# Performance work log

Measured on AMD Instinct MI355X. Metric: run time of the kernel, lower is better.

Reference implementation:

```python
import jax, jax.numpy as jnp
import numpy as np

N_NODES = 50000
N_EDGES = 800000
IN_CH = 128
HID = 64
HEADS = 4
OUT_CH = 10
N_GRAPHS = 512
NEG_SLOPE = 0.2


def setup_inputs() -> dict:
    key = jax.random.key(0)
    ks = jax.random.split(key, 16)
    x = jax.random.normal(ks[0], (N_NODES, IN_CH), dtype=jnp.float32)
    edge_index = jax.random.randint(ks[1], (2, N_EDGES), 0, N_NODES, dtype=jnp.int64)
    batch = jnp.sort(jax.random.randint(ks[2], (N_NODES,), 0, N_GRAPHS, dtype=jnp.int64))
    s = 1.0 / np.sqrt(IN_CH)
    W1 = jax.random.uniform(ks[3], (IN_CH, HEADS * HID), jnp.float32, -s, s)
    att_src1 = jax.random.normal(ks[4], (HEADS, HID), jnp.float32) * 0.1
    att_dst1 = jax.random.normal(ks[5], (HEADS, HID), jnp.float32) * 0.1
    b1 = jnp.zeros((HEADS * HID,), jnp.float32)
    s2 = 1.0 / np.sqrt(HEADS * HID)
    W2 = jax.random.uniform(ks[6], (HEADS * HID, HID), jnp.float32, -s2, s2)
    att_src2 = jax.random.normal(ks[7], (1, HID), jnp.float32) * 0.1
    att_dst2 = jax.random.normal(ks[8], (1, HID), jnp.float32) * 0.1
    b2 = jnp.zeros((HID,), jnp.float32)
    s3 = 1.0 / np.sqrt(HID)
    Wl = jax.random.uniform(ks[9], (HID, OUT_CH), jnp.float32, -s3, s3)
    bl = jnp.zeros((OUT_CH,), jnp.float32)
    return dict(x=x, edge_index=edge_index, batch=batch,
                W1=W1, att_src1=att_src1, att_dst1=att_dst1, b1=b1,
                W2=W2, att_src2=att_src2, att_dst2=att_dst2, b2=b2,
                Wl=Wl, bl=bl)


def gat_conv(x, src, dst, W, att_src, att_dst, bias, heads, out_ch, concat):
    """PyG GATConv: gather -> per-edge attention -> segment softmax over dst -> scatter-add."""
    n = x.shape[0]
    h = (x @ W).reshape(n, heads, out_ch)            # [N,H,C]
    a_s = jnp.sum(h * att_src, axis=-1)              # [N,H]
    a_d = jnp.sum(h * att_dst, axis=-1)              # [N,H]
    e = jax.nn.leaky_relu(a_s[src] + a_d[dst], NEG_SLOPE)  # [E,H]
    m = jax.ops.segment_max(e, dst, num_segments=n)  # stable softmax per dst
    alpha = jnp.exp(e - m[dst])
    denom = jax.ops.segment_sum(alpha, dst, num_segments=n)
    alpha = alpha / denom[dst]
    out = jax.ops.segment_sum(h[src] * alpha[:, :, None], dst, num_segments=n)  # [N,H,C]
    if concat:
        out = out.reshape(n, heads * out_ch)
    else:
        out = out.mean(axis=1)
    return out + bias


def reference(x, edge_index, batch, W1, att_src1, att_dst1, b1,
              W2, att_src2, att_dst2, b2, Wl, bl):
    n = x.shape[0]
    # PyG GATConv default add_self_loops=True
    loops = jnp.arange(n, dtype=edge_index.dtype)
    src = jnp.concatenate([edge_index[0], loops])
    dst = jnp.concatenate([edge_index[1], loops])

    h = jax.nn.elu(gat_conv(x, src, dst, W1, att_src1, att_dst1, b1, HEADS, HID, True))
    h = jax.nn.elu(gat_conv(h, src, dst, W2, att_src2, att_dst2, b2, 1, HID, False))

    # global_mean_pool
    sums = jax.ops.segment_sum(h, batch, num_segments=N_GRAPHS)
    cnts = jax.ops.segment_sum(jnp.ones((n,), h.dtype), batch, num_segments=N_GRAPHS)
    pooled = sums / jnp.maximum(cnts, 1.0)[:, None]

    return pooled @ Wl + bl
```

## Files before the change

kernel.cpp:

```cpp
#include <hip/hip_runtime.h>
#include <hip/hip_bf16.h>
#include <math.h>

#define N_NODES 50000
#define N_EDGES 800000
#define IN_CH 128
#define HID 64
#define HEADS 4
#define OUT_CH 10
#define N_GRAPHS 512
#define NEG_SLOPE 0.2f

#define ETOT_C (N_EDGES + N_NODES)
#define GB1 ((N_NODES + 63) / 64)
#define GH  ((ETOT_C / 4 + 255) / 256)
#define GZ  32

using short8_t = __attribute__((ext_vector_type(8))) short;
using f32x4 = __attribute__((ext_vector_type(4))) float;

__device__ __forceinline__ float b2f(unsigned short u) {
    return __uint_as_float(((unsigned)u) << 16);
}
__device__ __forceinline__ unsigned short f2b(float f) {
    __hip_bfloat16 b = __float2bfloat16(f);
    return *(unsigned short*)&b;
}
__device__ __forceinline__ short f2bs(float f) {
    __hip_bfloat16 b = __float2bfloat16(f);
    return *(short*)&b;
}
__device__ __forceinline__ float lrelu(float x) { return x > 0.f ? x : NEG_SLOPE * x; }

__global__ void convw_k(const float* __restrict__ W1, const float* __restrict__ W2,
                        unsigned short* __restrict__ Wt1, unsigned short* __restrict__ Wt2) {
    int idx = blockIdx.x * 256 + threadIdx.x;
    if (idx < 256 * 128) {
        int n = idx / 128, k = idx % 128;
        Wt1[idx] = f2b(W1[(size_t)k * 256 + n]);
    }
    int j = idx - 256 * 128;
    if (j >= 0 && j < 64 * 256) {
        int n = j / 256, k = j % 256;
        Wt2[j] = f2b(W2[(size_t)k * 64 + n]);
    }
}

__global__ __launch_bounds__(256) void mega1_k(
        const float* __restrict__ X, const unsigned short* __restrict__ Wt,
        unsigned short* __restrict__ Yb,
        const float* __restrict__ asrc, const float* __restrict__ adst,
        float* __restrict__ As, float* __restrict__ Ad, int M,
        const int* __restrict__ dst, int* __restrict__ deg, int* __restrict__ rank,
        const int* __restrict__ batch, float* __restrict__ cntf,
        float* __restrict__ pooled) {
    int b = blockIdx.x;
    if (b < GB1) {
        const int lane = threadIdx.x & 63;
        const int w = threadIdx.x >> 6;
        const int r0 = b * 64 + w * 16;
        const int l15 = lane & 15;
        const int rc = min(r0 + l15, M - 1);
        const int kg = (lane >> 4) * 8;

        f32x4 acc[16] = {};
#pragma unroll
        for (int kc = 0; kc < 4; kc++) {
            int k0 = kc * 32 + kg;
            float4 xa = *(const float4*)&X[(size_t)rc * 128 + k0];
            float4 xb = *(const float4*)&X[(size_t)rc * 128 + k0 + 4];
            short8_t af;
            af[0] = f2bs(xa.x); af[1] = f2bs(xa.y); af[2] = f2bs(xa.z); af[3] = f2bs(xa.w);
            af[4] = f2bs(xb.x); af[5] = f2bs(xb.y); af[6] = f2bs(xb.z); af[7] = f2bs(xb.w);
#pragma unroll
            for (int ct = 0; ct < 16; ct++) {
                int col = ct * 16 + l15;
                short8_t bf = *(const short8_t*)&Wt[(size_t)col * 128 + k0];
                acc[ct] = __builtin_amdgcn_mfma_f32_16x16x32_bf16(af, bf, acc[ct], 0, 0, 0);
            }
        }

        const int rbase = r0 + (lane >> 4) * 4;
#pragma unroll
        for (int reg = 0; reg < 4; reg++) {
            int gr = rbase + reg;
            float s0 = 0.f, s1 = 0.f, s2 = 0.f, s3 = 0.f;
            float d0 = 0.f, d1 = 0.f, d2 = 0.f, d3 = 0.f;
#pragma unroll
            for (int cg = 0; cg < 4; cg++) {
                int c = cg * 16 + l15;
                float v0 = acc[0 * 4 + cg][reg], v1 = acc[1 * 4 + cg][reg];
                float v2 = acc[2 * 4 + cg][reg], v3 = acc[3 * 4 + cg][reg];
                s0 += v0 * asrc[0 * 64 + c]; d0 += v0 * adst[0 * 64 + c];
                s1 += v1 * asrc[1 * 64 + c]; d1 += v1 * adst[1 * 64 + c];
                s2 += v2 * asrc[2 * 64 + c]; d2 += v2 * adst[2 * 64 + c];
                s3 += v3 * asrc[3 * 64 + c]; d3 += v3 * adst[3 * 64 + c];
            }
#pragma unroll
            for (int o = 8; o > 0; o >>= 1) {
                s0 += __shfl_xor(s0, o); d0 += __shfl_xor(d0, o);
                s1 += __shfl_xor(s1, o); d1 += __shfl_xor(d1, o);
                s2 += __shfl_xor(s2, o); d2 += __shfl_xor(d2, o);
                s3 += __shfl_xor(s3, o); d3 += __shfl_xor(d3, o);
            }
            if (l15 == 0 && gr < M) {
                *(float4*)&As[gr * 4] = make_float4(s0, s1, s2, s3);
                *(float4*)&Ad[gr * 4] = make_float4(d0, d1, d2, d3);
            }
        }
#pragma unroll
        for (int reg = 0; reg < 4; reg++) {
            int gr = rbase + reg;
            if (gr >= M) continue;
#pragma unroll
            for (int cg = 0; cg < 4; cg++) {
                int c = cg * 16 + l15;
                ushort4 p;
                p.x = f2b(acc[0 * 4 + cg][reg]);
                p.y = f2b(acc[1 * 4 + cg][reg]);
                p.z = f2b(acc[2 * 4 + cg][reg]);
                p.w = f2b(acc[3 * 4 + cg][reg]);
                *(ushort4*)&Yb[(size_t)gr * 256 + c * 4] = p;
            }
        }
        return;
    }
    b -= GB1;
    if (b < GH) {
        const int nth = GH * 256;
        int i0 = b * 256 + threadIdx.x;
        int i1 = i0 + nth, i2 = i0 + 2 * nth, i3 = i0 + 3 * nth;
        bool v0 = i0 < ETOT_C, v1 = i1 < ETOT_C, v2 = i2 < ETOT_C, v3 = i3 < ETOT_C;
        int d0 = 0, d1 = 0, d2 = 0, d3 = 0;
        if (v0) d0 = (i0 < N_EDGES) ? dst[i0] : i0 - N_EDGES;
        if (v1) d1 = (i1 < N_EDGES) ? dst[i1] : i1 - N_EDGES;
        if (v2) d2 = (i2 < N_EDGES) ? dst[i2] : i2 - N_EDGES;
        if (v3) d3 = (i3 < N_EDGES) ? dst[i3] : i3 - N_EDGES;
        int r0 = 0, r1 = 0, r2 = 0, r3 = 0;
        if (v0) r0 = atomicAdd(&deg[d0], 1);
        if (v1) r1 = atomicAdd(&deg[d1], 1);
        if (v2) r2 = atomicAdd(&deg[d2], 1);
        if (v3) r3 = atomicAdd(&deg[d3], 1);
        if (v0) rank[i0] = r0;
        if (v1) rank[i1] = r1;
        if (v2) rank[i2] = r2;
        if (v3) rank[i3] = r3;
        return;
    }
    b -= GH;
    if (b < 2) {
        int g = b * 256 + threadIdx.x;
        if (g >= N_GRAPHS) return;
        int lo = 0, hi = N_NODES;
        while (lo < hi) { int mid = (lo + hi) >> 1; if (batch[mid] < g) lo = mid + 1; else hi = mid; }
        int lo2 = lo, hi2 = N_NODES;
        while (lo2 < hi2) { int mid = (lo2 + hi2) >> 1; if (batch[mid] < g + 1) lo2 = mid + 1; else hi2 = mid; }
        cntf[g] = (float)(lo2 - lo);
        return;
    }
    b -= 2;
    int idx = b * 256 + threadIdx.x;
    *(float4*)&pooled[(size_t)idx * 4] = make_float4(0.f, 0.f, 0.f, 0.f);
}

__global__ __launch_bounds__(256) void mfma_gemm2_k(
        const unsigned short* __restrict__ Xb, const unsigned short* __restrict__ Wt,
        unsigned short* __restrict__ Yb,
        const float* __restrict__ asrc, const float* __restrict__ adst,
        float* __restrict__ As, float* __restrict__ Ad, int M) {
    const int lane = threadIdx.x & 63;
    const int w = threadIdx.x >> 6;
    const int r0 = blockIdx.x * 64 + w * 16;
    const int l15 = lane & 15;
    const int rc = min(r0 + l15, M - 1);
    const int kg = (lane >> 4) * 8;

    f32x4 acc[4] = {};
#pragma unroll
    for (int kc = 0; kc < 8; kc++) {
        int k0 = kc * 32 + kg;
        short8_t af = *(const short8_t*)&Xb[(size_t)rc * 256 + k0];
#pragma unroll
        for (int ct = 0; ct < 4; ct++) {
            int col = ct * 16 + l15;
            short8_t bf = *(const short8_t*)&Wt[(size_t)col * 256 + k0];
            acc[ct] = __builtin_amdgcn_mfma_f32_16x16x32_bf16(af, bf, acc[ct], 0, 0, 0);
        }
    }

    const int rbase = r0 + (lane >> 4) * 4;
#pragma unroll
    for (int reg = 0; reg < 4; reg++) {
        int gr = rbase + reg;
        float sv = 0.f, dv = 0.f;
#pragma unroll
        for (int ct = 0; ct < 4; ct++) {
            int c = ct * 16 + l15;
            float v = acc[ct][reg];
            sv += v * asrc[c];
            dv += v * adst[c];
        }
#pragma unroll
        for (int o = 8; o > 0; o >>= 1) { sv += __shfl_xor(sv, o); dv += __shfl_xor(dv, o); }
        if (l15 == 0 && gr < M) { As[gr] = sv; Ad[gr] = dv; }
        if (gr < M) {
#pragma unroll
            for (int ct = 0; ct < 4; ct++)
                Yb[(size_t)gr * 64 + ct * 16 + l15] = f2b(acc[ct][reg]);
        }
    }
}

__global__ void blksum_k(const int* __restrict__ deg, int* __restrict__ bsum, int n) {
    int t = threadIdx.x;
    int i = blockIdx.x * 256 + t;
    int v = (i < n) ? deg[i] : 0;
#pragma unroll
    for (int o = 32; o > 0; o >>= 1) v += __shfl_xor(v, o);
    __shared__ int wsum[4];
    if ((t & 63) == 0) wsum[t >> 6] = v;
    __syncthreads();
    if (t == 0) bsum[blockIdx.x] = wsum[0] + wsum[1] + wsum[2] + wsum[3];
}

__global__ void scanb_k(int* __restrict__ bsum, int nb) {
    __shared__ int tmp[256];
    int t = threadIdx.x;
    int v = (t < nb) ? bsum[t] : 0;
    tmp[t] = v;
    __syncthreads();
    for (int o = 1; o < 256; o <<= 1) {
        int u = (t >= o) ? tmp[t - o] : 0;
        __syncthreads();
        tmp[t] += u;
        __syncthreads();
    }
    if (t < nb) bsum[t] = tmp[t] - v;
}

__global__ void scanapply_k(const int* __restrict__ deg, const int* __restrict__ bsum,
                            int* __restrict__ rowptr, int n) {
    __shared__ int tmp[256];
    int t = threadIdx.x;
    int i = blockIdx.x * 256 + t;
    int v = (i < n) ? deg[i] : 0;
    tmp[t] = v;
    __syncthreads();
    for (int o = 1; o < 256; o <<= 1) {
        int u = (t >= o) ? tmp[t - o] : 0;
        __syncthreads();
        tmp[t] += u;
        __syncthreads();
    }
    int boff = bsum[blockIdx.x];
    if (i < n) rowptr[i] = boff + tmp[t] - v;
    if (i == n - 1) rowptr[n] = boff + tmp[t];
}

__global__ void scatter_k(const int* __restrict__ src, const int* __restrict__ dst,
                          const int* __restrict__ rowptr, const int* __restrict__ rank,
                          int* __restrict__ csrc, int etot) {
    int i = blockIdx.x * blockDim.x + threadIdx.x;
    if (i >= etot) return;
    int s, d;
    if (i < N_EDGES) { s = src[i]; d = dst[i]; } else { s = d = i - N_EDGES; }
    csrc[rowptr[d] + rank[i]] = s;
}

__global__ void agg1_k(const int* __restrict__ rowptr, const int* __restrict__ csrc,
                       const float* __restrict__ As, const float* __restrict__ Ad,
                       const __hip_bfloat16* __restrict__ Hb,
                       const float* __restrict__ bias,
                       unsigned short* __restrict__ Outb, int nnodes) {
    __shared__ int ssh[4][64];
    __shared__ float4 wsh[4][64];
    int lane = threadIdx.x & 63;
    int w = threadIdx.x >> 6;
    int node = blockIdx.x * 4 + w;
    int beg = rowptr[node], end = rowptr[node + 1];
    int deg = end - beg;
    const unsigned short* hb = (const unsigned short*)Hb;
    float4 bv = *(const float4*)&Ad[node * 4];
    bool fast = (deg <= 64);
    if (fast) {
        bool act = lane < deg;
        int s = act ? csrc[beg + lane] : 0;
        float4 a = *(const float4*)&As[s * 4];
        float e0 = lrelu(a.x + bv.x), e1 = lrelu(a.y + bv.y);
        float e2 = lrelu(a.z + bv.z), e3 = lrelu(a.w + bv.w);
        if (!act) { e0 = e1 = e2 = e3 = -INFINITY; }
        float m0 = e0, m1 = e1, m2 = e2, m3 = e3;
#pragma unroll
        for (int o = 32; o > 0; o >>= 1) {
            m0 = fmaxf(m0, __shfl_xor(m0, o)); m1 = fmaxf(m1, __shfl_xor(m1, o));
            m2 = fmaxf(m2, __shfl_xor(m2, o)); m3 = fmaxf(m3, __shfl_xor(m3, o));
        }
        float x0 = act ? __expf(e0 - m0) : 0.f;
        float x1 = act ? __expf(e1 - m1) : 0.f;
        float x2 = act ? __expf(e2 - m2) : 0.f;
        float x3 = act ? __expf(e3 - m3) : 0.f;
        float d0 = x0, d1 = x1, d2 = x2, d3 = x3;
#pragma unroll
        for (int o = 32; o > 0; o >>= 1) {
            d0 += __shfl_xor(d0, o); d1 += __shfl_xor(d1, o);
            d2 += __shfl_xor(d2, o); d3 += __shfl_xor(d3, o);
        }
        ssh[w][lane] = s;
        wsh[w][lane] = make_float4(x0 / d0, x1 / d1, x2 / d2, x3 / d3);
    }
    __syncthreads();
    float acc0 = 0.f, acc1 = 0.f, acc2 = 0.f, acc3 = 0.f;
    if (fast) {
        float p0 = 0.f, p1 = 0.f, p2 = 0.f, p3 = 0.f;
        int j = 0;
        for (; j + 4 <= deg; j += 4) {
            int sA = ssh[w][j], sB = ssh[w][j + 1], sC = ssh[w][j + 2], sD = ssh[w][j + 3];
            float4 wA = wsh[w][j], wB = wsh[w][j + 1], wC = wsh[w][j + 2], wD = wsh[w][j + 3];
            ushort4 vA = *(const ushort4*)&hb[(size_t)sA * 256 + lane * 4];
            ushort4 vB = *(const ushort4*)&hb[(size_t)sB * 256 + lane * 4];
            ushort4 vC = *(const ushort4*)&hb[(size_t)sC * 256 + lane * 4];
            ushort4 vD = *(const ushort4*)&hb[(size_t)sD * 256 + lane * 4];
            acc0 += wA.x * b2f(vA.x) + wC.x * b2f(vC.x);
            p0   += wB.x * b2f(vB.x) + wD.x * b2f(vD.x);
            acc1 += wA.y * b2f(vA.y) + wC.y * b2f(vC.y);
            p1   += wB.y * b2f(vB.y) + wD.y * b2f(vD.y);
            acc2 += wA.z * b2f(vA.z) + wC.z * b2f(vC.z);
            p2   += wB.z * b2f(vB.z) + wD.z * b2f(vD.z);
            acc3 += wA.w * b2f(vA.w) + wC.w * b2f(vC.w);
            p3   += wB.w * b2f(vB.w) + wD.w * b2f(vD.w);
        }
        for (; j < deg; j++) {
            int s = ssh[w][j];
            float4 wt = wsh[w][j];
            ushort4 v = *(const ushort4*)&hb[(size_t)s * 256 + lane * 4];
            acc0 += wt.x * b2f(v.x); acc1 += wt.y * b2f(v.y);
            acc2 += wt.z * b2f(v.z); acc3 += wt.w * b2f(v.w);
        }
        acc0 += p0; acc1 += p1; acc2 += p2; acc3 += p3;
    } else {
        float m0 = -INFINITY, m1 = -INFINITY, m2 = -INFINITY, m3 = -INFINITY;
        for (int j = beg + lane; j < end; j += 64) {
            float4 a = *(const float4*)&As[csrc[j] * 4];
            m0 = fmaxf(m0, lrelu(a.x + bv.x)); m1 = fmaxf(m1, lrelu(a.y + bv.y));
            m2 = fmaxf(m2, lrelu(a.z + bv.z)); m3 = fmaxf(m3, lrelu(a.w + bv.w));
        }
#pragma unroll
        for (int o = 32; o > 0; o >>= 1) {
            m0 = fmaxf(m0, __shfl_xor(m0, o)); m1 = fmaxf(m1, __shfl_xor(m1, o));
            m2 = fmaxf(m2, __shfl_xor(m2, o)); m3 = fmaxf(m3, __shfl_xor(m3, o));
        }
        float d0 = 0.f, d1 = 0.f, d2 = 0.f, d3 = 0.f;
        for (int j = beg + lane; j < end; j += 64) {
            float4 a = *(const float4*)&As[csrc[j] * 4];
            d0 += __expf(lrelu(a.x + bv.x) - m0); d1 += __expf(lrelu(a.y + bv.y) - m1);
            d2 += __expf(lrelu(a.z + bv.z) - m2); d3 += __expf(lrelu(a.w + bv.w) - m3);
        }
#pragma unroll
        for (int o = 32; o > 0; o >>= 1) {
            d0 += __shfl_xor(d0, o); d1 += __shfl_xor(d1, o);
            d2 += __shfl_xor(d2, o); d3 += __shfl_xor(d3, o);
        }
        for (int j = beg; j < end; j++) {
            int s = csrc[j];
            float4 a = *(const float4*)&As[s * 4];
            float w0 = __expf(lrelu(a.x + bv.x) - m0) / d0;
            float w1 = __expf(lrelu(a.y + bv.y) - m1) / d1;
            float w2 = __expf(lrelu(a.z + bv.z) - m2) / d2;
            float w3 = __expf(lrelu(a.w + bv.w) - m3) / d3;
            ushort4 v = *(const ushort4*)&hb[(size_t)s * 256 + lane * 4];
            acc0 += w0 * b2f(v.x); acc1 += w1 * b2f(v.y);
            acc2 += w2 * b2f(v.z); acc3 += w3 * b2f(v.w);
        }
    }
    float r0 = acc0 + bias[0 * 64 + lane];
    float r1 = acc1 + bias[1 * 64 + lane];
    float r2 = acc2 + bias[2 * 64 + lane];
    float r3 = acc3 + bias[3 * 64 + lane];
    r0 = r0 > 0.f ? r0 : expm1f(r0);
    r1 = r1 > 0.f ? r1 : expm1f(r1);
    r2 = r2 > 0.f ? r2 : expm1f(r2);
    r3 = r3 > 0.f ? r3 : expm1f(r3);
    size_t base = (size_t)node * 256;
    Outb[base + 0 * 64 + lane] = f2b(r0);
    Outb[base + 1 * 64 + lane] = f2b(r1);
    Outb[base + 2 * 64 + lane] = f2b(r2);
    Outb[base + 3 * 64 + lane] = f2b(r3);
}

__global__ void agg2_k(const int* __restrict__ rowptr, const int* __restrict__ csrc,
                       const float* __restrict__ As, const float* __restrict__ Ad,
                       const __hip_bfloat16* __restrict__ Hb,
                       const float* __restrict__ bias, const int* __restrict__ batch,
                       float* __restrict__ pooled, int nnodes) {
    __shared__ int ssh[4][64];
    __shared__ float wsh[4][64];
    int lane = threadIdx.x & 63;
    int w = threadIdx.x >> 6;
    int node = blockIdx.x * 4 + w;
    int beg = rowptr[node], end = rowptr[node + 1];
    int deg = end - beg;
    const unsigned short* hb = (const unsigned short*)Hb;
    float ad = Ad[node];
    bool fast = (deg <= 64);
    if (fast) {
        bool act = lane < deg;
        int s = act ? csrc[beg + lane] : 0;
        float e = lrelu(As[s] + ad);
        if (!act) e = -INFINITY;
        float m = e;
#pragma unroll
        for (int o = 32; o > 0; o >>= 1) m = fmaxf(m, __shfl_xor(m, o));
        float x = act ? __expf(e - m) : 0.f;
        float d = x;
#pragma unroll
        for (int o = 32; o > 0; o >>= 1) d += __shfl_xor(d, o);
        ssh[w][lane] = s;
        wsh[w][lane] = x / d;
    }
    __syncthreads();
    float acc = 0.f;
    if (fast) {
        float p = 0.f;
        int j = 0;
        for (; j + 4 <= deg; j += 4) {
            int sA = ssh[w][j], sB = ssh[w][j + 1], sC = ssh[w][j + 2], sD = ssh[w][j + 3];
            float wA = wsh[w][j], wB = wsh[w][j + 1], wC = wsh[w][j + 2], wD = wsh[w][j + 3];
            acc += wA * b2f(hb[(size_t)sA * 64 + lane]) + wC * b2f(hb[(size_t)sC * 64 + lane]);
            p   += wB * b2f(hb[(size_t)sB * 64 + lane]) + wD * b2f(hb[(size_t)sD * 64 + lane]);
        }
        for (; j < deg; j++) acc += wsh[w][j] * b2f(hb[(size_t)ssh[w][j] * 64 + lane]);
        acc += p;
    } else {
        float m = -INFINITY;
        for (int j = beg + lane; j < end; j += 64) m = fmaxf(m, lrelu(As[csrc[j]] + ad));
#pragma unroll
        for (int o = 32; o > 0; o >>= 1) m = fmaxf(m, __shfl_xor(m, o));
        float d = 0.f;
        for (int j = beg + lane; j < end; j += 64) d += __expf(lrelu(As[csrc[j]] + ad) - m);
#pragma unroll
        for (int o = 32; o > 0; o >>= 1) d += __shfl_xor(d, o);
        for (int j = beg; j < end; j++) {
            int s = csrc[j];
            float wt = __expf(lrelu(As[s] + ad) - m) / d;
            acc += wt * b2f(hb[(size_t)s * 64 + lane]);
        }
    }
    float v = acc + bias[lane];
    v = v > 0.f ? v : expm1f(v);
    atomicAdd(&pooled[batch[node] * 64 + lane], v);
}

__global__ void final_k(const float* __restrict__ pooled, const float* __restrict__ cnt,
                        const float* __restrict__ Wl, const float* __restrict__ bl,
                        float* __restrict__ out) {
    int g = blockIdx.x;
    int t = threadIdx.x;
    __shared__ float s[64];
    float c = cnt[g];
    c = c > 1.f ? c : 1.f;
    s[t] = pooled[g * 64 + t] / c;
    __syncthreads();
    if (t < OUT_CH) {
        float acc = bl[t];
        for (int k = 0; k < 64; k++) acc += s[k] * Wl[k * OUT_CH + t];
        out[g * OUT_CH + t] = acc;
    }
}

extern "C" void kernel_launch(void* const* d_in, const int* in_sizes, int n_in,
                              void* d_out, int out_size, void* d_ws, size_t ws_size,
                              hipStream_t stream) {
    const float* x    = (const float*)d_in[0];
    const int*   ei   = (const int*)d_in[1];
    const int*   batch= (const int*)d_in[2];
    const float* W1   = (const float*)d_in[3];
    const float* as1  = (const float*)d_in[4];
    const float* ad1  = (const float*)d_in[5];
    const float* b1   = (const float*)d_in[6];
    const float* W2   = (const float*)d_in[7];
    const float* as2  = (const float*)d_in[8];
    const float* ad2  = (const float*)d_in[9];
    const float* b2   = (const float*)d_in[10];
    const float* Wl   = (const float*)d_in[11];
    const float* bl   = (const float*)d_in[12];
    float* out = (float*)d_out;

    const int* src = ei;
    const int* dst = ei + N_EDGES;
    const int ETOT = ETOT_C;
    const int NB = (N_NODES + 255) / 256;

    char* ws = (char*)d_ws;
    size_t off = 0;
    auto alloc = [&](size_t bytes) {
        void* p = ws + off;
        off = (off + bytes + 255) & ~((size_t)255);
        return p;
    };
    unsigned short* h1b  = (unsigned short*)alloc((size_t)N_NODES * 256 * 2);
    unsigned short* out1b= (unsigned short*)alloc((size_t)N_NODES * 256 * 2);
    float* As1    = (float*)alloc((size_t)N_NODES * 4 * 4);
    float* Ad1    = (float*)alloc((size_t)N_NODES * 4 * 4);
    float* As2    = (float*)alloc((size_t)N_NODES * 4);
    float* Ad2    = (float*)alloc((size_t)N_NODES * 4);
    int*   deg    = (int*)  alloc((size_t)N_NODES * 4);
    int*   rowptr = (int*)  alloc((size_t)(N_NODES + 1) * 4);
    int*   csrc   = (int*)  alloc((size_t)ETOT * 4);
    int*   rank   = (int*)  alloc((size_t)ETOT * 4);
    int*   bsum   = (int*)  alloc((size_t)NB * 4);
    unsigned short* Wt1 = (unsigned short*)alloc((size_t)256 * 128 * 2);
    unsigned short* Wt2 = (unsigned short*)alloc((size_t)64 * 256 * 2);
    float* pooled = (float*)alloc((size_t)N_GRAPHS * 64 * 4);
    float* cntf   = (float*)alloc((size_t)N_GRAPHS * 4);
    unsigned short* h2b = h1b;

    hipMemsetAsync(deg, 0, (size_t)N_NODES * 4, stream);

    convw_k<<<192, 256, 0, stream>>>(W1, W2, Wt1, Wt2);
    mega1_k<<<GB1 + GH + 2 + GZ, 256, 0, stream>>>(
        x, Wt1, h1b, as1, ad1, As1, Ad1, N_NODES,
        dst, deg, rank, batch, cntf, pooled);

    blksum_k<<<NB, 256, 0, stream>>>(deg, bsum, N_NODES);
    scanb_k<<<1, 256, 0, stream>>>(bsum, NB);
    scanapply_k<<<NB, 256, 0, stream>>>(deg, bsum, rowptr, N_NODES);
    scatter_k<<<(ETOT + 255) / 256, 256, 0, stream>>>(src, dst, rowptr, rank, csrc, ETOT);

    agg1_k<<<N_NODES / 4, 256, 0, stream>>>(rowptr, csrc, As1, Ad1,
                                            (const __hip_bfloat16*)h1b, b1, out1b, N_NODES);

    mfma_gemm2_k<<<(N_NODES + 63) / 64, 256, 0, stream>>>(out1b, Wt2, h2b, as2, ad2,
                                                          As2, Ad2, N_NODES);
    agg2_k<<<N_NODES / 4, 256, 0, stream>>>(rowptr, csrc, As2, Ad2,
                                            (const __hip_bfloat16*)h2b, b2, batch, pooled, N_NODES);

    final_k<<<N_GRAPHS, 64, 0, stream>>>(pooled, cntf, Wl, bl, out);
}
```

Measured before the change: 234.6 us.

## Build CSR via two-level bucketed counting sort with shared-memory histograms

Replaces the per-edge global atomic degree/rank counting, three-kernel scan and random scatter with a two-pass bucket sort. Edges are first histogrammed into 128-node buckets in shared memory, then scattered into bucket-contiguous (src,dst) pairs, and finally each bucket is locally sorted per node to produce rowptr and csrc. The aim is to cut global atomic contention and random global writes, in exchange for an extra int2 intermediate buffer and more kernel passes. The order of sources within a node is now nondeterministic, which can change floating-point summation order.

```diff
diff --git a/kernel.cpp b/kernel.cpp
--- a/kernel.cpp
+++ b/kernel.cpp
@@ -12,9 +12,12 @@
 #define NEG_SLOPE 0.2f
 
 #define ETOT_C (N_EDGES + N_NODES)
+#define NPB 128
+#define NBUK ((N_NODES + NPB - 1) / NPB)
+#define EPB 2048
+#define GA ((ETOT_C + EPB - 1) / EPB)
 #define GB1 ((N_NODES + 63) / 64)
-#define GH  ((ETOT_C / 4 + 255) / 256)
-#define GZ  32
+#define GZ 32
 
 using short8_t = __attribute__((ext_vector_type(8))) short;
 using f32x4 = __attribute__((ext_vector_type(4))) float;
@@ -51,7 +54,7 @@
         unsigned short* __restrict__ Yb,
         const float* __restrict__ asrc, const float* __restrict__ adst,
         float* __restrict__ As, float* __restrict__ Ad, int M,
-        const int* __restrict__ dst, int* __restrict__ deg, int* __restrict__ rank,
+        const int* __restrict__ dst, unsigned* __restrict__ bcnt,
         const int* __restrict__ batch, float* __restrict__ cntf,
         float* __restrict__ pooled) {
     int b = blockIdx.x;
@@ -126,28 +129,23 @@
         return;
     }
     b -= GB1;
-    if (b < GH) {
-        const int nth = GH * 256;
-        int i0 = b * 256 + threadIdx.x;
-        int i1 = i0 + nth, i2 = i0 + 2 * nth, i3 = i0 + 3 * nth;
-        bool v0 = i0 < ETOT_C, v1 = i1 < ETOT_C, v2 = i2 < ETOT_C, v3 = i3 < ETOT_C;
-        int d0 = 0, d1 = 0, d2 = 0, d3 = 0;
-        if (v0) d0 = (i0 < N_EDGES) ? dst[i0] : i0 - N_EDGES;
-        if (v1) d1 = (i1 < N_EDGES) ? dst[i1] : i1 - N_EDGES;
-        if (v2) d2 = (i2 < N_EDGES) ? dst[i2] : i2 - N_EDGES;
-        if (v3) d3 = (i3 < N_EDGES) ? dst[i3] : i3 - N_EDGES;
-        int r0 = 0, r1 = 0, r2 = 0, r3 = 0;
-        if (v0) r0 = atomicAdd(&deg[d0], 1);
-        if (v1) r1 = atomicAdd(&deg[d1], 1);
-        if (v2) r2 = atomicAdd(&deg[d2], 1);
-        if (v3) r3 = atomicAdd(&deg[d3], 1);
-        if (v0) rank[i0] = r0;
-        if (v1) rank[i1] = r1;
-        if (v2) rank[i2] = r2;
-        if (v3) rank[i3] = r3;
+    if (b < GA) {
+        __shared__ unsigned bins[NBUK];
+        int t = threadIdx.x;
+        for (int i = t; i < NBUK; i += 256) bins[i] = 0;
+        __syncthreads();
+        int e0 = b * EPB;
+        int e1 = min(e0 + EPB, ETOT_C);
+        for (int i = e0 + t; i < e1; i += 256) {
+            int d = (i < N_EDGES) ? dst[i] : i - N_EDGES;
+            atomicAdd(&bins[d >> 7], 1u);
+        }
+        __syncthreads();
+        for (int i = t; i < NBUK; i += 256)
+            if (bins[i]) atomicAdd(&bcnt[i], bins[i]);
         return;
     }
-    b -= GH;
+    b -= GA;
     if (b < 2) {
         int g = b * 256 + threadIdx.x;
         if (g >= N_GRAPHS) return;
@@ -161,6 +159,100 @@
     b -= 2;
     int idx = b * 256 + threadIdx.x;
     *(float4*)&pooled[(size_t)idx * 4] = make_float4(0.f, 0.f, 0.f, 0.f);
+}
+
+__global__ void scanB_k(const unsigned* __restrict__ bcnt, int* __restrict__ bbase,
+                        unsigned* __restrict__ bcur) {
+    __shared__ int tmp[512];
+    int t = threadIdx.x;
+    int v = (t < NBUK) ? (int)bcnt[t] : 0;
+    tmp[t] = v;
+    __syncthreads();
+    for (int o = 1; o < 512; o <<= 1) {
+        int u = (t >= o) ? tmp[t - o] : 0;
+        __syncthreads();
+        tmp[t] += u;
+        __syncthreads();
+    }
+    if (t < NBUK) {
+        int ex = tmp[t] - v;
+        bbase[t] = ex;
+        bcur[t] = (unsigned)ex;
+    }
+    if (t == NBUK - 1) bbase[NBUK] = tmp[t];
+}
+
+__global__ __launch_bounds__(256) void passB_k(const int* __restrict__ src,
+                                               const int* __restrict__ dst,
+                                               unsigned* __restrict__ bcur,
+                                               int2* __restrict__ ebuf) {
+    __shared__ unsigned bins[NBUK];
+    __shared__ unsigned bbl[NBUK];
+    __shared__ int dstash[EPB];
+    int b = blockIdx.x;
+    int t = threadIdx.x;
+    for (int i = t; i < NBUK; i += 256) bins[i] = 0;
+    __syncthreads();
+    int e0 = b * EPB;
+    int e1 = min(e0 + EPB, ETOT_C);
+    for (int i = e0 + t; i < e1; i += 256) {
+        int d = (i < N_EDGES) ? dst[i] : i - N_EDGES;
+        dstash[i - e0] = d;
+        atomicAdd(&bins[d >> 7], 1u);
+    }
+    __syncthreads();
+    for (int i = t; i < NBUK; i += 256) {
+        bbl[i] = bins[i] ? atomicAdd(&bcur[i], bins[i]) : 0u;
+    }
+    __syncthreads();
+    for (int i = t; i < NBUK; i += 256) bins[i] = 0;
+    __syncthreads();
+    for (int i = e0 + t; i < e1; i += 256) {
+        int d = dstash[i - e0];
+        int s = (i < N_EDGES) ? src[i] : i - N_EDGES;
+        unsigned r = atomicAdd(&bins[d >> 7], 1u);
+        ebuf[bbl[d >> 7] + r] = make_int2(s, d);
+    }
+}
+
+__global__ __launch_bounds__(256) void passC_k(const int* __restrict__ bbase,
+                                               const int2* __restrict__ ebuf,
+                                               int* __restrict__ rowptr,
+                                               int* __restrict__ csrc) {
+    __shared__ int cnt[NPB];
+    __shared__ int loc[NPB];
+    __shared__ int cur[NPB];
+    int b = blockIdx.x;
+    int t = threadIdx.x;
+    int base = bbase[b], end = bbase[b + 1];
+    if (t < NPB) cnt[t] = 0;
+    __syncthreads();
+    for (int j = base + t; j < end; j += 256) {
+        int2 e = ebuf[j];
+        atomicAdd(&cnt[e.y & (NPB - 1)], 1);
+    }
+    __syncthreads();
+    if (t < NPB) loc[t] = cnt[t];
+    __syncthreads();
+    for (int o = 1; o < NPB; o <<= 1) {
+        int v = (t < NPB && t >= o) ? loc[t - o] : 0;
+        __syncthreads();
+        if (t < NPB) loc[t] += v;
+        __syncthreads();
+    }
+    if (t < NPB) {
+        int node = b * NPB + t;
+        if (node < N_NODES) rowptr[node] = base + loc[t] - cnt[t];
+        cur[t] = 0;
+    }
+    if (b == NBUK - 1 && t == 0) rowptr[N_NODES] = end;
+    __syncthreads();
+    for (int j = base + t; j < end; j += 256) {
+        int2 e = ebuf[j];
+        int n = e.y & (NPB - 1);
+        int r = atomicAdd(&cur[n], 1);
+        csrc[base + loc[n] - cnt[n] + r] = e.x;
+    }
 }
 
 __global__ __launch_bounds__(256) void mfma_gemm2_k(
@@ -209,62 +301,6 @@
                 Yb[(size_t)gr * 64 + ct * 16 + l15] = f2b(acc[ct][reg]);
         }
     }
-}
-
-__global__ void blksum_k(const int* __restrict__ deg, int* __restrict__ bsum, int n) {
-    int t = threadIdx.x;
-    int i = blockIdx.x * 256 + t;
-    int v = (i < n) ? deg[i] : 0;
-#pragma unroll
-    for (int o = 32; o > 0; o >>= 1) v += __shfl_xor(v, o);
-    __shared__ int wsum[4];
-    if ((t & 63) == 0) wsum[t >> 6] = v;
-    __syncthreads();
-    if (t == 0) bsum[blockIdx.x] = wsum[0] + wsum[1] + wsum[2] + wsum[3];
-}
-
-__global__ void scanb_k(int* __restrict__ bsum, int nb) {
-    __shared__ int tmp[256];
-    int t = threadIdx.x;
-    int v = (t < nb) ? bsum[t] : 0;
-    tmp[t] = v;
-    __syncthreads();
-    for (int o = 1; o < 256; o <<= 1) {
-        int u = (t >= o) ? tmp[t - o] : 0;
-        __syncthreads();
-        tmp[t] += u;
-        __syncthreads();
-    }
-    if (t < nb) bsum[t] = tmp[t] - v;
-}
-
-__global__ void scanapply_k(const int* __restrict__ deg, const int* __restrict__ bsum,
-                            int* __restrict__ rowptr, int n) {
-    __shared__ int tmp[256];
-    int t = threadIdx.x;
-    int i = blockIdx.x * 256 + t;
-    int v = (i < n) ? deg[i] : 0;
-    tmp[t] = v;
-    __syncthreads();
-    for (int o = 1; o < 256; o <<= 1) {
-        int u = (t >= o) ? tmp[t - o] : 0;
-        __syncthreads();
-        tmp[t] += u;
-        __syncthreads();
-    }
-    int boff = bsum[blockIdx.x];
-    if (i < n) rowptr[i] = boff + tmp[t] - v;
-    if (i == n - 1) rowptr[n] = boff + tmp[t];
-}
-
-__global__ void scatter_k(const int* __restrict__ src, const int* __restrict__ dst,
-                          const int* __restrict__ rowptr, const int* __restrict__ rank,
-                          int* __restrict__ csrc, int etot) {
-    int i = blockIdx.x * blockDim.x + threadIdx.x;
-    if (i >= etot) return;
-    int s, d;
-    if (i < N_EDGES) { s = src[i]; d = dst[i]; } else { s = d = i - N_EDGES; }
-    csrc[rowptr[d] + rank[i]] = s;
 }
 
 __global__ void agg1_k(const int* __restrict__ rowptr, const int* __restrict__ csrc,
@@ -487,8 +523,6 @@
 
     const int* src = ei;
     const int* dst = ei + N_EDGES;
-    const int ETOT = ETOT_C;
-    const int NB = (N_NODES + 255) / 256;
 
     char* ws = (char*)d_ws;
     size_t off = 0;
@@ -503,28 +537,28 @@
     float* Ad1    = (float*)alloc((size_t)N_NODES * 4 * 4);
     float* As2    = (float*)alloc((size_t)N_NODES * 4);
     float* Ad2    = (float*)alloc((size_t)N_NODES * 4);
-    int*   deg    = (int*)  alloc((size_t)N_NODES * 4);
     int*   rowptr = (int*)  alloc((size_t)(N_NODES + 1) * 4);
-    int*   csrc   = (int*)  alloc((size_t)ETOT * 4);
-    int*   rank   = (int*)  alloc((size_t)ETOT * 4);
-    int*   bsum   = (int*)  alloc((size_t)NB * 4);
+    int*   csrc   = (int*)  alloc((size_t)ETOT_C * 4);
+    int2*  ebuf   = (int2*) alloc((size_t)ETOT_C * 8);
+    unsigned* bcnt= (unsigned*)alloc((size_t)NBUK * 4);
+    int*   bbase  = (int*)  alloc((size_t)(NBUK + 1) * 4);
+    unsigned* bcur= (unsigned*)alloc((size_t)NBUK * 4);
     unsigned short* Wt1 = (unsigned short*)alloc((size_t)256 * 128 * 2);
     unsigned short* Wt2 = (unsigned short*)alloc((size_t)64 * 256 * 2);
     float* pooled = (float*)alloc((size_t)N_GRAPHS * 64 * 4);
     float* cntf   = (float*)alloc((size_t)N_GRAPHS * 4);
     unsigned short* h2b = h1b;
 
-    hipMemsetAsync(deg, 0, (size_t)N_NODES * 4, stream);
+    hipMemsetAsync(bcnt, 0, (size_t)NBUK * 4, stream);
 
     convw_k<<<192, 256, 0, stream>>>(W1, W2, Wt1, Wt2);
-    mega1_k<<<GB1 + GH + 2 + GZ, 256, 0, stream>>>(
+    mega1_k<<<GB1 + GA + 2 + GZ, 256, 0, stream>>>(
         x, Wt1, h1b, as1, ad1, As1, Ad1, N_NODES,
-        dst, deg, rank, batch, cntf, pooled);
-
-    blksum_k<<<NB, 256, 0, stream>>>(deg, bsum, N_NODES);
-    scanb_k<<<1, 256, 0, stream>>>(bsum, NB);
-    scanapply_k<<<NB, 256, 0, stream>>>(deg, bsum, rowptr, N_NODES);
-    scatter_k<<<(ETOT + 255) / 256, 256, 0, stream>>>(src, dst, rowptr, rank, csrc, ETOT);
+        dst, bcnt, batch, cntf, pooled);
+
+    scanB_k<<<1, 512, 0, stream>>>(bcnt, bbase, bcur);
+    passB_k<<<GA, 256, 0, stream>>>(src, dst, bcur, ebuf);
+    passC_k<<<NBUK, 256, 0, stream>>>(bbase, ebuf, rowptr, csrc);
 
     agg1_k<<<N_NODES / 4, 256, 0, stream>>>(rowptr, csrc, As1, Ad1,
                                             (const __hip_bfloat16*)h1b, b1, out1b, N_NODES);
```

Result: faster. 219.3 us (-6.5%).
